# Kernel optimization log

Measured on AMD Instinct MI355X. Metric: run time of the kernel, lower is better.

Reference implementation:

```python
import jax, jax.numpy as jnp
import numpy as np

F_BINS = 12
T_STEPS = 15
N = F_BINS * T_STEPS  # 180 patches
C = 768
R = C // 4            # 192 reduced dim for Q/K
B = 256
LN_EPS = 1e-5


def _build_physical_adjacency():
    A = np.zeros((N, N), dtype=np.float32)
    for f in range(F_BINS):
        for t in range(T_STEPS):
            i = f * T_STEPS + t
            if t < T_STEPS - 1:
                j = f * T_STEPS + (t + 1)
                A[i, j] = 1.0
                A[j, i] = 1.0
            hf = f * 2 + 1
            if hf < F_BINS:
                j = hf * T_STEPS + t
                A[i, j] = 1.0
                A[j, i] = 1.0
    A = A / (A.sum(axis=1, keepdims=True) + 1e-8)
    return jnp.asarray(A)


def setup_inputs() -> dict:
    key = jax.random.key(0)
    ks = jax.random.split(key, 8)
    x = jax.random.normal(ks[0], (B, N, C), dtype=jnp.float32)
    Wq = jax.random.normal(ks[1], (C, R), dtype=jnp.float32) * 0.02
    bq = jnp.zeros((R,), dtype=jnp.float32)
    Wk = jax.random.normal(ks[2], (C, R), dtype=jnp.float32) * 0.02
    bk = jnp.zeros((R,), dtype=jnp.float32)
    Wg = jax.random.normal(ks[3], (C, C), dtype=jnp.float32) * 0.02
    bg = jnp.zeros((C,), dtype=jnp.float32)
    gamma = jnp.ones((C,), dtype=jnp.float32)
    beta = jnp.zeros((C,), dtype=jnp.float32)
    alpha = jnp.asarray(0.8, dtype=jnp.float32)
    A_phys = _build_physical_adjacency()
    return {"x": x, "Wq": Wq, "bq": bq, "Wk": Wk, "bk": bk,
            "Wg": Wg, "bg": bg, "gamma": gamma, "beta": beta,
            "alpha": alpha, "A_phys": A_phys}


def reference(x, Wq, bq, Wk, bk, Wg, bg, gamma, beta, alpha, A_phys):
    # Q/K projections: [B,N,R]
    Q = jnp.einsum('bnc,cr->bnr', x, Wq) + bq
    K = jnp.einsum('bnc,cr->bnr', x, Wk) + bk
    # Dynamic adjacency: scaled dot-product softmax over nodes.
    scores = jnp.einsum('bnr,bmr->bnm', Q, K) / jnp.sqrt(jnp.asarray(R, x.dtype))
    A_dyn = jax.nn.softmax(scores, axis=-1)  # dropout is identity in eval
    a = jax.nn.sigmoid(alpha)
    A_comb = a * A_phys[None, :, :] + (1.0 - a) * A_dyn
    # GCN aggregation + projection
    z = jnp.einsum('bnm,bmc->bnc', A_comb, x)
    z = jnp.einsum('bnc,cd->bnd', z, Wg) + bg
    h = x + jax.nn.relu(z)
    # LayerNorm over channel dim
    mu = jnp.mean(h, axis=-1, keepdims=True)
    var = jnp.mean((h - mu) ** 2, axis=-1, keepdims=True)
    out = (h - mu) * jax.lax.rsqrt(var + LN_EPS) * gamma + beta
    return out
```

## Files before the change

kernel.cpp:

```cpp
#include <hip/hip_runtime.h>
#include <hip/hip_bf16.h>
#include <math.h>
#include <stdint.h>

#define BB   256
#define NN   180
#define CC   768
#define RR   192
#define MROWS (BB*NN)
#define KPAD 192

typedef __attribute__((ext_vector_type(8))) __bf16 bf16x8;
typedef __attribute__((ext_vector_type(4))) __bf16 bf16x4;
typedef __attribute__((ext_vector_type(4))) float  floatx4;

__device__ __forceinline__ void gload_lds16(const __bf16* g, __bf16* lds)
{
    __builtin_amdgcn_global_load_lds(
        (const __attribute__((address_space(1))) void*)(uintptr_t)(const void*)g,
        (__attribute__((address_space(3))) void*)(uintptr_t)(void*)lds,
        16, 0, 0);
}

template<int MODE>
__global__ __launch_bounds__(256) void gemm128(
    const __bf16* __restrict__ A,  int lda, long sAb,
    const __bf16* __restrict__ Bt, int ldb, long sBb,
    void* __restrict__ Cout, int ldc, long sCb,
    int M, int N, int K,
    const float* __restrict__ bias,
    const float* __restrict__ scale,
    const float* __restrict__ addx)
{
    const int z = blockIdx.z;
    const __bf16* Ab = A  + (long)z * sAb;
    const __bf16* Bb = Bt + (long)z * sBb;
    const int m0 = blockIdx.y * 128;
    const int n0 = blockIdx.x * 128;
    const int t  = threadIdx.x;
    const int w  = t >> 6;
    const int l  = t & 63;
    const int lr = l & 15;
    const int q  = l >> 4;

    __shared__ __align__(16) __bf16 sa[2][128 * 32];
    __shared__ __align__(16) __bf16 sb[2][128 * 32];

    floatx4 acc[4][4] = {};

    const int wm = (w & 1) * 64;
    const int wn = (w >> 1) * 64;

    const int srow = l >> 2;
    const int skc  = (l & 3) * 8;

    int arow0 = m0 + w * 16 + srow;        if (arow0 > M - 1) arow0 = M - 1;
    int arow1 = m0 + (w + 4) * 16 + srow;  if (arow1 > M - 1) arow1 = M - 1;
    int brow0 = n0 + w * 16 + srow;        if (brow0 > N - 1) brow0 = N - 1;
    int brow1 = n0 + (w + 4) * 16 + srow;  if (brow1 > N - 1) brow1 = N - 1;

    const __bf16* agp0 = Ab + (long)arow0 * lda + skc;
    const __bf16* agp1 = Ab + (long)arow1 * lda + skc;
    const __bf16* bgp0 = Bb + (long)brow0 * ldb + skc;
    const __bf16* bgp1 = Bb + (long)brow1 * ldb + skc;

    auto issue = [&](int buf, int k0) {
        gload_lds16(agp0 + k0, &sa[buf][(size_t)w * 512]);
        gload_lds16(agp1 + k0, &sa[buf][(size_t)(w + 4) * 512]);
        gload_lds16(bgp0 + k0, &sb[buf][(size_t)w * 512]);
        gload_lds16(bgp1 + k0, &sb[buf][(size_t)(w + 4) * 512]);
    };

    auto compute = [&](int buf) {
        bf16x8 af[4], bfv[4];
#pragma unroll
        for (int i = 0; i < 4; ++i)
            af[i] = *reinterpret_cast<const bf16x8*>(&sa[buf][(wm + i * 16 + lr) * 32 + q * 8]);
#pragma unroll
        for (int j = 0; j < 4; ++j)
            bfv[j] = *reinterpret_cast<const bf16x8*>(&sb[buf][(wn + j * 16 + lr) * 32 + q * 8]);
#pragma unroll
        for (int i = 0; i < 4; ++i)
#pragma unroll
            for (int j = 0; j < 4; ++j)
                acc[i][j] = __builtin_amdgcn_mfma_f32_16x16x32_bf16(af[i], bfv[j], acc[i][j], 0, 0, 0);
    };

    issue(0, 0);
    __syncthreads();
    for (int k0 = 0; k0 < K; k0 += 64) {
        issue(1, k0 + 32);
        compute(0);
        __syncthreads();
        if (k0 + 64 < K) issue(0, k0 + 64);
        compute(1);
        __syncthreads();
    }

#pragma unroll
    for (int i = 0; i < 4; ++i) {
        const int mbase = m0 + wm + i * 16 + q * 4;
#pragma unroll
        for (int j = 0; j < 4; ++j) {
            const int n = n0 + wn + j * 16 + lr;
#pragma unroll
            for (int r = 0; r < 4; ++r) {
                const int m = mbase + r;
                if (m < M && n < N) {
                    float v = acc[i][j][r];
                    if (MODE == 0) {
                        v = (v + bias[n]) * scale[n];
                        ((__bf16*)Cout)[(long)z * sCb + (long)m * ldc + n] = (__bf16)v;
                    } else if (MODE == 1) {
                        ((__bf16*)Cout)[(long)z * sCb + (long)m * ldc + n] = (__bf16)v;
                    } else {
                        v = v + bias[n];
                        v = v > 0.f ? v : 0.f;
                        v += addx[(long)m * ldc + n];
                        ((float*)Cout)[(long)m * ldc + n] = v;
                    }
                }
            }
        }
    }
}

__global__ __launch_bounds__(256) void convert_x(const float4* __restrict__ x4,
                                                 __bf16* __restrict__ xb, int n4)
{
    int i = blockIdx.x * 256 + threadIdx.x;
    int stride = gridDim.x * 256;
    for (; i < n4; i += stride) {
        float4 v = x4[i];
        bf16x4 o;
        o[0] = (__bf16)v.x; o[1] = (__bf16)v.y; o[2] = (__bf16)v.z; o[3] = (__bf16)v.w;
        *reinterpret_cast<bf16x4*>(xb + 4 * (long)i) = o;
    }
}

__global__ __launch_bounds__(256) void prep_weights(
    const float* __restrict__ Wq, const float* __restrict__ bq,
    const float* __restrict__ Wk, const float* __restrict__ bk,
    const float* __restrict__ Wg,
    __bf16* __restrict__ WqkT, __bf16* __restrict__ WgT,
    float* __restrict__ biasqk, float* __restrict__ scaleqk)
{
    int blk = blockIdx.x, t = threadIdx.x;
    if (blk < 384) {
        int n = blk;
        const float* W = (n < RR) ? Wq : Wk;
        int nn = (n < RR) ? n : n - RR;
        for (int k = t; k < CC; k += 256)
            WqkT[(long)n * CC + k] = (__bf16)W[(long)k * RR + nn];
        if (blk == 0) {
            for (int i = t; i < 384; i += 256) {
                biasqk[i]  = (i < RR) ? bq[i] : bk[i - RR];
                scaleqk[i] = (i < RR) ? rsqrtf((float)RR) : 1.0f;
            }
        }
    } else {
        int n = blk - 384;
        for (int k = t; k < CC; k += 256)
            WgT[(long)n * CC + k] = (__bf16)Wg[(long)k * CC + n];
    }
}

__global__ __launch_bounds__(256) void transpose_x(const __bf16* __restrict__ xb,
                                                   __bf16* __restrict__ xbT)
{
    const int c0 = (blockIdx.x % 12) * 64;
    const int b  = blockIdx.x / 12;
    __shared__ __bf16 lds[64 * 194];
    const int t = threadIdx.x;

    for (int i = 0; i < 45; ++i) {
        int idx = i * 256 + t;
        int m = idx >> 6, c = idx & 63;
        lds[c * 194 + m] = xb[((long)(b * NN + m)) * CC + c0 + c];
    }
    __syncthreads();
    for (int j = 0; j < 48; ++j) {
        int idx = j * 256 + t;
        int c = idx / KPAD, m = idx % KPAD;
        __bf16 v = (m < NN) ? lds[c * 194 + m] : (__bf16)0.0f;
        xbT[((long)(b * CC + c0 + c)) * KPAD + m] = v;
    }
}

__global__ __launch_bounds__(256) void softmax_combine(
    const __bf16* __restrict__ S, const float* __restrict__ A_phys,
    const float* __restrict__ alpha, __bf16* __restrict__ Acomb)
{
    const int w = threadIdx.x >> 6, l = threadIdx.x & 63;
    const long row = (long)blockIdx.x * 4 + w;
    const int b = (int)(row / NN), n = (int)(row % NN);
    const __bf16* Srow = S + ((long)b * NN + n) * NN;

    float v[3];
#pragma unroll
    for (int i = 0; i < 3; ++i) {
        int m = l + 64 * i;
        v[i] = (m < NN) ? (float)Srow[m] : -1e30f;
    }
    float mx = fmaxf(fmaxf(v[0], v[1]), v[2]);
    for (int off = 32; off; off >>= 1) mx = fmaxf(mx, __shfl_xor(mx, off, 64));

    float e[3], sum = 0.f;
#pragma unroll
    for (int i = 0; i < 3; ++i) {
        int m = l + 64 * i;
        e[i] = (m < NN) ? expf(v[i] - mx) : 0.f;
        sum += e[i];
    }
    for (int off = 32; off; off >>= 1) sum += __shfl_xor(sum, off, 64);

    const float a   = 1.f / (1.f + expf(-alpha[0]));
    const float inv = (1.f - a) / sum;
    __bf16* Orow = Acomb + ((long)b * NN + n) * KPAD;
#pragma unroll
    for (int i = 0; i < 3; ++i) {
        int m = l + 64 * i;
        if (m < KPAD) {
            float o = (m < NN) ? (a * A_phys[n * NN + m] + e[i] * inv) : 0.f;
            Orow[m] = (__bf16)o;
        }
    }
}

__global__ __launch_bounds__(256) void ln_kernel(float* __restrict__ out,
                                                 const float* __restrict__ gamma,
                                                 const float* __restrict__ beta)
{
    float* p = out + (long)blockIdx.x * CC;
    const int t = threadIdx.x, w = t >> 6, l = t & 63;
    float h[3], s = 0.f, s2 = 0.f;
#pragma unroll
    for (int i = 0; i < 3; ++i) {
        h[i] = p[t + 256 * i];
        s += h[i]; s2 += h[i] * h[i];
    }
    for (int off = 32; off; off >>= 1) { s += __shfl_xor(s, off, 64); s2 += __shfl_xor(s2, off, 64); }
    __shared__ float ps[4], ps2[4];
    if (l == 0) { ps[w] = s; ps2[w] = s2; }
    __syncthreads();
    s  = ps[0] + ps[1] + ps[2] + ps[3];
    s2 = ps2[0] + ps2[1] + ps2[2] + ps2[3];
    const float mu  = s * (1.f / CC);
    const float var = s2 * (1.f / CC) - mu * mu;
    const float rs  = rsqrtf(var + 1e-5f);
#pragma unroll
    for (int i = 0; i < 3; ++i) {
        int c = t + 256 * i;
        p[c] = (h[i] - mu) * rs * gamma[c] + beta[c];
    }
}

extern "C" void kernel_launch(void* const* d_in, const int* in_sizes, int n_in,
                              void* d_out, int out_size, void* d_ws, size_t ws_size,
                              hipStream_t stream)
{
    const float* x      = (const float*)d_in[0];
    const float* Wq     = (const float*)d_in[1];
    const float* bq     = (const float*)d_in[2];
    const float* Wk     = (const float*)d_in[3];
    const float* bk     = (const float*)d_in[4];
    const float* Wg     = (const float*)d_in[5];
    const float* bg     = (const float*)d_in[6];
    const float* gamma  = (const float*)d_in[7];
    const float* beta   = (const float*)d_in[8];
    const float* alpha  = (const float*)d_in[9];
    const float* A_phys = (const float*)d_in[10];

    char* w = (char*)d_ws;
    __bf16* xb    = (__bf16*)(w + 0);
    __bf16* zbuf  = xb;
    __bf16* xbT   = (__bf16*)(w + 70778880);
    __bf16* QK    = (__bf16*)(w + 146276352);
    __bf16* Acomb = QK;
    __bf16* S     = (__bf16*)(w + 181665792);
    __bf16* WqkT  = (__bf16*)(w + 198254592);
    __bf16* WgT   = (__bf16*)(w + 198844416);
    float*  biasqk  = (float*)(w + 200024064);
    float*  scaleqk = (float*)(w + 200025600);

    convert_x<<<4096, 256, 0, stream>>>((const float4*)x, xb, MROWS * CC / 4);
    prep_weights<<<384 + CC, 256, 0, stream>>>(Wq, bq, Wk, bk, Wg, WqkT, WgT, biasqk, scaleqk);
    transpose_x<<<BB * 12, 256, 0, stream>>>(xb, xbT);

    gemm128<0><<<dim3(384 / 128, MROWS / 128, 1), 256, 0, stream>>>(
        xb, CC, 0L, WqkT, CC, 0L, QK, 384, 0L,
        MROWS, 384, CC, biasqk, scaleqk, nullptr);

    gemm128<1><<<dim3(2, 2, BB), 256, 0, stream>>>(
        QK, 384, (long)NN * 384, QK + RR, 384, (long)NN * 384,
        S, NN, (long)NN * NN,
        NN, NN, RR, nullptr, nullptr, nullptr);

    softmax_combine<<<MROWS / 4, 256, 0, stream>>>(S, A_phys, alpha, Acomb);

    gemm128<1><<<dim3(CC / 128, 2, BB), 256, 0, stream>>>(
        Acomb, KPAD, (long)NN * KPAD, xbT, KPAD, (long)CC * KPAD,
        zbuf, CC, (long)NN * CC,
        NN, CC, KPAD, nullptr, nullptr, nullptr);

    gemm128<3><<<dim3(CC / 128, MROWS / 128, 1), 256, 0, stream>>>(
        zbuf, CC, 0L, WgT, CC, 0L, d_out, CC, 0L,
        MROWS, CC, CC, bg, nullptr, x);

    ln_kernel<<<MROWS, 256, 0, stream>>>((float*)d_out, gamma, beta);
}
```

Measured before the change: 680.2 us.

## Fuse x conversion with transpose, swizzle GEMM LDS, remap workgroups across XCDs

Merges the fp32-to-bf16 conversion and the per-batch transpose into one kernel, so x no longer takes an extra bf16 write-then-read round trip. In the GEMM, the k-chunk column used for global-to-LDS stores and fragment reads is XOR-swizzled to cut LDS bank conflicts. The flattened workgroup index is also remapped so consecutive tiles land on the same XCD, aiming for better L2 reuse. The fused kernel writes scalar bf16 values into LDS with a transposed stride, which may cause bank conflicts of its own.

Result: no change. 667.2 us (-1.9%).

```diff
diff --git a/kernel.cpp b/kernel.cpp
--- a/kernel.cpp
+++ b/kernel.cpp
@@ -35,13 +35,20 @@
     const int z = blockIdx.z;
     const __bf16* Ab = A  + (long)z * sAb;
     const __bf16* Bb = Bt + (long)z * sBb;
-    const int m0 = blockIdx.y * 128;
-    const int n0 = blockIdx.x * 128;
+
+    const int nwg = gridDim.x * gridDim.y;
+    const int lin = blockIdx.y * gridDim.x + blockIdx.x;
+    const int qd = nwg >> 3, rr = nwg & 7, xc = lin & 7, oo = lin >> 3;
+    const int wg = (xc < rr ? xc * (qd + 1) : rr * (qd + 1) + (xc - rr) * qd) + oo;
+    const int m0 = (wg / gridDim.x) * 128;
+    const int n0 = (wg % gridDim.x) * 128;
+
     const int t  = threadIdx.x;
     const int w  = t >> 6;
     const int l  = t & 63;
     const int lr = l & 15;
     const int q  = l >> 4;
+    const int xr = (lr >> 1) & 3;
 
     __shared__ __align__(16) __bf16 sa[2][128 * 32];
     __shared__ __align__(16) __bf16 sb[2][128 * 32];
@@ -52,7 +59,7 @@
     const int wn = (w >> 1) * 64;
 
     const int srow = l >> 2;
-    const int skc  = (l & 3) * 8;
+    const int skc  = ((l & 3) ^ ((l >> 3) & 3)) * 8;
 
     int arow0 = m0 + w * 16 + srow;        if (arow0 > M - 1) arow0 = M - 1;
     int arow1 = m0 + (w + 4) * 16 + srow;  if (arow1 > M - 1) arow1 = M - 1;
@@ -75,10 +82,12 @@
         bf16x8 af[4], bfv[4];
 #pragma unroll
         for (int i = 0; i < 4; ++i)
-            af[i] = *reinterpret_cast<const bf16x8*>(&sa[buf][(wm + i * 16 + lr) * 32 + q * 8]);
+            af[i] = *reinterpret_cast<const bf16x8*>(
+                &sa[buf][(wm + i * 16 + lr) * 32 + ((q ^ xr) * 8)]);
 #pragma unroll
         for (int j = 0; j < 4; ++j)
-            bfv[j] = *reinterpret_cast<const bf16x8*>(&sb[buf][(wn + j * 16 + lr) * 32 + q * 8]);
+            bfv[j] = *reinterpret_cast<const bf16x8*>(
+                &sb[buf][(wn + j * 16 + lr) * 32 + ((q ^ xr) * 8)]);
 #pragma unroll
         for (int i = 0; i < 4; ++i)
 #pragma unroll
@@ -125,16 +134,36 @@
     }
 }
 
-__global__ __launch_bounds__(256) void convert_x(const float4* __restrict__ x4,
-                                                 __bf16* __restrict__ xb, int n4)
-{
-    int i = blockIdx.x * 256 + threadIdx.x;
-    int stride = gridDim.x * 256;
-    for (; i < n4; i += stride) {
-        float4 v = x4[i];
-        bf16x4 o;
-        o[0] = (__bf16)v.x; o[1] = (__bf16)v.y; o[2] = (__bf16)v.z; o[3] = (__bf16)v.w;
-        *reinterpret_cast<bf16x4*>(xb + 4 * (long)i) = o;
+__global__ __launch_bounds__(256) void convert_transpose_x(
+    const float* __restrict__ x, __bf16* __restrict__ xb, __bf16* __restrict__ xbT)
+{
+    const int c0 = (blockIdx.x % 12) * 64;
+    const int b  = blockIdx.x / 12;
+    __shared__ __bf16 lds[64 * 194];
+    const int t = threadIdx.x;
+
+    for (int i = 0; i < 12; ++i) {
+        int idx = i * 256 + t;
+        if (idx < 2880) {
+            int m = idx >> 4, c4 = idx & 15;
+            float4 v = *reinterpret_cast<const float4*>(
+                &x[((long)(b * NN + m)) * CC + c0 + c4 * 4]);
+            bf16x4 o;
+            o[0] = (__bf16)v.x; o[1] = (__bf16)v.y;
+            o[2] = (__bf16)v.z; o[3] = (__bf16)v.w;
+            *reinterpret_cast<bf16x4*>(&xb[((long)(b * NN + m)) * CC + c0 + c4 * 4]) = o;
+            lds[(c4 * 4 + 0) * 194 + m] = o[0];
+            lds[(c4 * 4 + 1) * 194 + m] = o[1];
+            lds[(c4 * 4 + 2) * 194 + m] = o[2];
+            lds[(c4 * 4 + 3) * 194 + m] = o[3];
+        }
+    }
+    __syncthreads();
+    for (int j = 0; j < 48; ++j) {
+        int idx = j * 256 + t;
+        int c = idx / KPAD, m = idx % KPAD;
+        __bf16 v = (m < NN) ? lds[c * 194 + m] : (__bf16)0.0f;
+        xbT[((long)(b * CC + c0 + c)) * KPAD + m] = v;
     }
 }
 
@@ -165,28 +194,6 @@
     }
 }
 
-__global__ __launch_bounds__(256) void transpose_x(const __bf16* __restrict__ xb,
-                                                   __bf16* __restrict__ xbT)
-{
-    const int c0 = (blockIdx.x % 12) * 64;
-    const int b  = blockIdx.x / 12;
-    __shared__ __bf16 lds[64 * 194];
-    const int t = threadIdx.x;
-
-    for (int i = 0; i < 45; ++i) {
-        int idx = i * 256 + t;
-        int m = idx >> 6, c = idx & 63;
-        lds[c * 194 + m] = xb[((long)(b * NN + m)) * CC + c0 + c];
-    }
-    __syncthreads();
-    for (int j = 0; j < 48; ++j) {
-        int idx = j * 256 + t;
-        int c = idx / KPAD, m = idx % KPAD;
-        __bf16 v = (m < NN) ? lds[c * 194 + m] : (__bf16)0.0f;
-        xbT[((long)(b * CC + c0 + c)) * KPAD + m] = v;
-    }
-}
-
 __global__ __launch_bounds__(256) void softmax_combine(
     const __bf16* __restrict__ S, const float* __restrict__ A_phys,
     const float* __restrict__ alpha, __bf16* __restrict__ Acomb)
@@ -283,9 +290,8 @@
     float*  biasqk  = (float*)(w + 200024064);
     float*  scaleqk = (float*)(w + 200025600);
 
-    convert_x<<<4096, 256, 0, stream>>>((const float4*)x, xb, MROWS * CC / 4);
     prep_weights<<<384 + CC, 256, 0, stream>>>(Wq, bq, Wk, bk, Wg, WqkT, WgT, biasqk, scaleqk);
-    transpose_x<<<BB * 12, 256, 0, stream>>>(xb, xbT);
+    convert_transpose_x<<<BB * 12, 256, 0, stream>>>(x, xb, xbT);
 
     gemm128<0><<<dim3(384 / 128, MROWS / 128, 1), 256, 0, stream>>>(
         xb, CC, 0L, WqkT, CC, 0L, QK, 384, 0L,
```
